# Kernel optimization log

Measured on AMD Instinct MI355X. Metric: run time of the kernel, lower is better.

The kernel has to match this reference:

```python
import jax, jax.numpy as jnp
import numpy as np

B, C, E = 2, 1024, 1024
H = 16            # n_heads as declared (used as per-group feature dim due to module's reshape)
HD = E // H       # 64 — the axis actually batched over in attention


def setup_inputs() -> dict:
    key = jax.random.key(0)
    ks = jax.random.split(key, 5)
    scale = 0.02
    return {
        "x": jax.random.normal(ks[0], (B, C, E), dtype=jnp.float32),
        "W_q": jax.random.normal(ks[1], (E, E), dtype=jnp.float32) * scale,
        "W_k": jax.random.normal(ks[2], (E, E), dtype=jnp.float32) * scale,
        "W_v": jax.random.normal(ks[3], (E, E), dtype=jnp.float32) * scale,
        "W_o": jax.random.normal(ks[4], (E, E), dtype=jnp.float32) * scale,
    }


def reference(x, W_q, W_k, W_v, W_o):
    # nn.Linear: y = x @ W.T  (bias=False)
    def proj_split(W):
        y = jnp.einsum('bce,de->bcd', x, W)              # [B,C,E]
        # view(B, C, HD, H).transpose(1,2) -> [B, HD, C, H]  (faithful to source layout)
        return y.reshape(B, C, HD, H).transpose(0, 2, 1, 3)

    Q = proj_split(W_q)
    K = proj_split(W_k)
    V = proj_split(W_v)

    scale = 1.0 / jnp.sqrt(jnp.asarray(H, dtype=x.dtype))  # sqrt of last dim (= n_heads here)
    scores = jnp.einsum('bdqh,bdkh->bdqk', Q, K) * scale    # [B, HD, C, C]
    weights = jax.nn.softmax(scores, axis=-1)
    out = jnp.einsum('bdqk,bdkh->bdqh', weights, V)         # [B, HD, C, H]
    out = out.transpose(0, 2, 1, 3).reshape(B, C, E)        # [B, C, E]
    out = jnp.einsum('bce,de->bcd', out, W_o)
    return out  # dropout p=0.0 / eval mode: identity
```

## Files before the change

### kernel.cpp

```cpp
#include <hip/hip_runtime.h>
#include <stdint.h>
#include <math.h>


typedef __bf16   bf16x8 __attribute__((ext_vector_type(8)));
typedef float    f32x4  __attribute__((ext_vector_type(4)));

__device__ __forceinline__ unsigned short f2bf(float f) {
    unsigned int u = __float_as_uint(f);
    u += 0x7FFFu + ((u >> 16) & 1u);
    return (unsigned short)(u >> 16);
}

__device__ __forceinline__ void gl16(const unsigned short* g, unsigned short* l) {
    __builtin_amdgcn_global_load_lds(
        (const __attribute__((address_space(1))) unsigned int*)g,
        (__attribute__((address_space(3))) unsigned int*)l, 16, 0, 0);
}

__global__ __launch_bounds__(256) void cast_to_bf16(
    const float* __restrict__ x,
    const float* __restrict__ w0, const float* __restrict__ w1,
    const float* __restrict__ w2, const float* __restrict__ w3,
    unsigned short* __restrict__ xb,
    unsigned short* __restrict__ b0, unsigned short* __restrict__ b1,
    unsigned short* __restrict__ b2, unsigned short* __restrict__ b3)
{
    const int z = blockIdx.y;
    const float* src;
    unsigned short* dst;
    size_t off = 0;
    float sc = 1.f;
    if (z < 2)       { src = x;  dst = xb; off = (size_t)z << 20; }
    else if (z == 2) { src = w0; dst = b0; sc = 0.36067376022224085f; }
    else if (z == 3) { src = w1; dst = b1; }
    else if (z == 4) { src = w2; dst = b2; }
    else             { src = w3; dst = b3; }
    const size_t i = off + ((size_t)blockIdx.x * 256 + threadIdx.x) * 4;
    const float4 v = *(const float4*)(src + i);
    *(ushort4*)(dst + i) = make_ushort4(f2bf(v.x * sc), f2bf(v.y * sc),
                                        f2bf(v.z * sc), f2bf(v.w * sc));
}

__global__ __launch_bounds__(256) void gemm128_bt_mfma(
    const unsigned short* __restrict__ A,
    const unsigned short* __restrict__ B0, const unsigned short* __restrict__ B1,
    const unsigned short* __restrict__ B2,
    unsigned short* __restrict__ C0, unsigned short* __restrict__ C1,
    unsigned short* __restrict__ C2,
    int M, int N, int K)
{
    const unsigned short* Bm = (blockIdx.z == 0) ? B0 : (blockIdx.z == 1) ? B1 : B2;
    unsigned short* Cm       = (blockIdx.z == 0) ? C0 : (blockIdx.z == 1) ? C1 : C2;

    __shared__ __align__(16) unsigned short As[2][128 * 32];
    __shared__ __align__(16) unsigned short Bs[2][128 * 32];

    const int t    = threadIdx.x;
    const int lane = t & 63;
    const int w    = t >> 6;
    const int m0   = blockIdx.y * 128;
    const int n0   = blockIdx.x * 128;
    const int wm   = (w & 1) * 64;
    const int wn   = (w >> 1) * 64;

    const int r0 = t >> 2;
    const int c0 = (t & 3) * 8;
    const unsigned short* Apa = A  + (size_t)(m0 + r0) * K + c0;
    const unsigned short* Apb = Apa + (size_t)64 * K;
    const unsigned short* Bpa = Bm + (size_t)(n0 + r0) * K + c0;
    const unsigned short* Bpb = Bpa + (size_t)64 * K;
    unsigned short* lA0 = &As[0][w * 512];
    unsigned short* lA1 = &As[0][2048 + w * 512];
    unsigned short* lB0 = &Bs[0][w * 512];
    unsigned short* lB1 = &Bs[0][2048 + w * 512];
    const int bufStr = 128 * 32;

    f32x4 acc[4][4];
#pragma unroll
    for (int i = 0; i < 4; ++i)
#pragma unroll
        for (int j = 0; j < 4; ++j) acc[i][j] = (f32x4){0.f, 0.f, 0.f, 0.f};

    const int fm = lane & 15;
    const int kg = lane >> 4;

    gl16(Apa, lA0);
    gl16(Apb, lA1);
    gl16(Bpa, lB0);
    gl16(Bpb, lB1);

    int cur = 0;
    for (int k0 = 0; k0 < K; k0 += 32) {
        __syncthreads();

        if (k0 + 32 < K) {
            const int nb = (cur ^ 1);
            gl16(Apa + k0 + 32, lA0 + nb * bufStr);
            gl16(Apb + k0 + 32, lA1 + nb * bufStr);
            gl16(Bpa + k0 + 32, lB0 + nb * bufStr);
            gl16(Bpb + k0 + 32, lB1 + nb * bufStr);
        }

        const unsigned short* Ab = &As[cur][0];
        const unsigned short* Bb = &Bs[cur][0];
        bf16x8 af[4], bfr[4];
#pragma unroll
        for (int im = 0; im < 4; ++im)
            af[im] = *(const bf16x8*)&Ab[(wm + im * 16 + fm) * 32 + kg * 8];
#pragma unroll
        for (int in = 0; in < 4; ++in)
            bfr[in] = *(const bf16x8*)&Bb[(wn + in * 16 + fm) * 32 + kg * 8];
#pragma unroll
        for (int im = 0; im < 4; ++im)
#pragma unroll
            for (int in = 0; in < 4; ++in)
                acc[im][in] = __builtin_amdgcn_mfma_f32_16x16x32_bf16(
                    af[im], bfr[in], acc[im][in], 0, 0, 0);

        cur ^= 1;
    }

#pragma unroll
    for (int im = 0; im < 4; ++im) {
#pragma unroll
        for (int in = 0; in < 4; ++in) {
            const int row = m0 + wm + im * 16 + kg * 4;
            const int col = n0 + wn + in * 16 + fm;
#pragma unroll
            for (int r = 0; r < 4; ++r)
                Cm[(size_t)(row + r) * N + col] = f2bf(acc[im][in][r]);
        }
    }
}

__global__ __launch_bounds__(256) void gemm64_bt_mfma(
    const unsigned short* __restrict__ A, const unsigned short* __restrict__ Bm,
    float* __restrict__ Cm, int M, int N, int K)
{
    __shared__ __align__(16) unsigned short As[2][64 * 32];
    __shared__ __align__(16) unsigned short Bs[2][64 * 32];

    const int t    = threadIdx.x;
    const int lane = t & 63;
    const int w    = t >> 6;
    const int m0   = blockIdx.y * 64;
    const int n0   = blockIdx.x * 64;
    const int wm   = (w & 1) * 32;
    const int wn   = (w >> 1) * 32;

    const int r0 = t >> 2;
    const int c0 = (t & 3) * 8;
    const unsigned short* Apa = A  + (size_t)(m0 + r0) * K + c0;
    const unsigned short* Bpa = Bm + (size_t)(n0 + r0) * K + c0;
    unsigned short* ldsA = &As[0][w * 512];
    unsigned short* ldsB = &Bs[0][w * 512];
    const int bufStr = 64 * 32;

    f32x4 acc[2][2];
#pragma unroll
    for (int i = 0; i < 2; ++i)
#pragma unroll
        for (int j = 0; j < 2; ++j) acc[i][j] = (f32x4){0.f, 0.f, 0.f, 0.f};

    const int fm = lane & 15;
    const int kg = lane >> 4;

    gl16(Apa, ldsA);
    gl16(Bpa, ldsB);

    int cur = 0;
    for (int k0 = 0; k0 < K; k0 += 32) {
        __syncthreads();

        if (k0 + 32 < K) {
            const int nb = (cur ^ 1);
            gl16(Apa + k0 + 32, ldsA + nb * bufStr);
            gl16(Bpa + k0 + 32, ldsB + nb * bufStr);
        }

        const unsigned short* Ab = &As[cur][0];
        const unsigned short* Bb = &Bs[cur][0];
        bf16x8 af[2], bfr[2];
#pragma unroll
        for (int im = 0; im < 2; ++im)
            af[im] = *(const bf16x8*)&Ab[(wm + im * 16 + fm) * 32 + kg * 8];
#pragma unroll
        for (int in = 0; in < 2; ++in)
            bfr[in] = *(const bf16x8*)&Bb[(wn + in * 16 + fm) * 32 + kg * 8];
#pragma unroll
        for (int im = 0; im < 2; ++im)
#pragma unroll
            for (int in = 0; in < 2; ++in)
                acc[im][in] = __builtin_amdgcn_mfma_f32_16x16x32_bf16(
                    af[im], bfr[in], acc[im][in], 0, 0, 0);

        cur ^= 1;
    }

#pragma unroll
    for (int im = 0; im < 2; ++im) {
#pragma unroll
        for (int in = 0; in < 2; ++in) {
            const int row = m0 + wm + im * 16 + kg * 4;
            const int col = n0 + wn + in * 16 + fm;
#pragma unroll
            for (int r = 0; r < 4; ++r)
                Cm[(size_t)(row + r) * N + col] = acc[im][in][r];
        }
    }
}

#define KROWS 40
#define VROWS 72

__global__ __launch_bounds__(256, 4) void attn_mfma(
    const unsigned short* __restrict__ Qb, const unsigned short* __restrict__ Kb,
    const unsigned short* __restrict__ Vb, unsigned short* __restrict__ Ob)
{
    __shared__ __align__(16) unsigned char smem[34816];

    const int t    = threadIdx.x;
    const int lane = t & 63;
    const int wv   = t >> 6;
    const int fm   = lane & 15;
    const int kg   = lane >> 4;

    const int blk = blockIdx.x;
    const int xcd = blk & 7;
    const int i_  = blk >> 3;
    const int qt  = i_ & 7;
    const int hdg = (i_ >> 3) & 3;
    const int gs  = (i_ >> 5) & 1;
    const int bb  = (i_ >> 6) & 1;
    const int hd  = (xcd + gs * 8) * 4 + hdg;
    const size_t base = ((size_t)bb << 20) + (size_t)hd * 16;
    const int q0 = qt * 128;
    const int wk = wv * 32;

    unsigned short* Ks  = (unsigned short*)(smem + wv * 2560);
    unsigned short* VsT = (unsigned short*)(smem + 10240 + wv * 2304);
    float*          Red = (float*)smem;

    const int key2 = lane >> 1, half = lane & 1;
    const int vcol = ((key2 & 15) >> 2) * 8 + (key2 & 3) + ((key2 >> 4) << 2);

    union { uint4 u; bf16x8 h; } zz; zz.u = make_uint4(0, 0, 0, 0);
    bf16x8 aq[8];
#pragma unroll
    for (int m = 0; m < 8; ++m) {
        if (kg < 2)
            aq[m] = *(const bf16x8*)(Qb + base +
                     (size_t)(q0 + m * 16 + fm) * 1024 + kg * 8);
        else
            aq[m] = zz.h;
    }

    f32x4 oacc[8];
    float lp[8];
#pragma unroll
    for (int m = 0; m < 8; ++m) {
        oacc[m] = (f32x4){0.f, 0.f, 0.f, 0.f};
        lp[m] = 0.f;
    }

    uint4 kd = *(const uint4*)(Kb + base + (size_t)(wk + key2) * 1024 + half * 8);
    uint4 vd = *(const uint4*)(Vb + base + (size_t)(wk + key2) * 1024 + half * 8);

    for (int kt = 0; kt < 1024; kt += 128) {
        {
            *(uint4*)&Ks[key2 * KROWS + half * 8] = kd;
            const unsigned short* pv = (const unsigned short*)&vd;
#pragma unroll
            for (int d = 0; d < 8; ++d)
                VsT[(half * 8 + d) * VROWS + vcol] = pv[d];
        }

        bf16x8 bk0 = zz.h, bk1 = zz.h;
        if (kg < 2) {
            bk0 = *(const bf16x8*)&Ks[fm * KROWS + kg * 8];
            bk1 = *(const bf16x8*)&Ks[(16 + fm) * KROWS + kg * 8];
        }

        const bf16x8 bv = *(const bf16x8*)&VsT[fm * VROWS + kg * 8];

        if (kt + 128 < 1024) {
            kd = *(const uint4*)(Kb + base +
                  (size_t)(kt + 128 + wk + key2) * 1024 + half * 8);
            vd = *(const uint4*)(Vb + base +
                  (size_t)(kt + 128 + wk + key2) * 1024 + half * 8);
        }

#pragma unroll
        for (int m = 0; m < 8; ++m) {
            f32x4 s0 = __builtin_amdgcn_mfma_f32_16x16x32_bf16(
                bk0, aq[m], (f32x4){0.f, 0.f, 0.f, 0.f}, 0, 0, 0);
            f32x4 s1 = __builtin_amdgcn_mfma_f32_16x16x32_bf16(
                bk1, aq[m], (f32x4){0.f, 0.f, 0.f, 0.f}, 0, 0, 0);
            const float p0 = __builtin_amdgcn_exp2f(s0[0]);
            const float p1 = __builtin_amdgcn_exp2f(s0[1]);
            const float p2 = __builtin_amdgcn_exp2f(s0[2]);
            const float p3 = __builtin_amdgcn_exp2f(s0[3]);
            const float p4 = __builtin_amdgcn_exp2f(s1[0]);
            const float p5 = __builtin_amdgcn_exp2f(s1[1]);
            const float p6 = __builtin_amdgcn_exp2f(s1[2]);
            const float p7 = __builtin_amdgcn_exp2f(s1[3]);
            lp[m] += ((p0 + p1) + (p2 + p3)) + ((p4 + p5) + (p6 + p7));
            bf16x8 aph;
            aph[0] = (__bf16)p0; aph[1] = (__bf16)p1;
            aph[2] = (__bf16)p2; aph[3] = (__bf16)p3;
            aph[4] = (__bf16)p4; aph[5] = (__bf16)p5;
            aph[6] = (__bf16)p6; aph[7] = (__bf16)p7;
            oacc[m] = __builtin_amdgcn_mfma_f32_16x16x32_bf16(
                aph, bv, oacc[m], 0, 0, 0);
        }
    }

#pragma unroll
    for (int m = 0; m < 8; ++m) {
        lp[m] += __shfl_xor(lp[m], 16, 64);
        lp[m] += __shfl_xor(lp[m], 32, 64);
    }

    __syncthreads();
#pragma unroll
    for (int m = 0; m < 8; ++m) {
#pragma unroll
        for (int r = 0; r < 4; ++r)
            Red[((wv * 128) + m * 16 + kg * 4 + r) * 17 + fm] = oacc[m][r];
        if (kg == 0)
            Red[((wv * 128) + m * 16 + fm) * 17 + 16] = lp[m];
    }
    __syncthreads();

#pragma unroll
    for (int mp = 0; mp < 2; ++mp) {
#pragma unroll
        for (int r = 0; r < 4; ++r) {
            const int q = wv * 32 + mp * 16 + kg * 4 + r;
            const float o = Red[q * 17 + fm]         + Red[(128 + q) * 17 + fm] +
                            Red[(256 + q) * 17 + fm] + Red[(384 + q) * 17 + fm];
            const float l = Red[q * 17 + 16]         + Red[(128 + q) * 17 + 16] +
                            Red[(256 + q) * 17 + 16] + Red[(384 + q) * 17 + 16];
            Ob[base + (size_t)(q0 + q) * 1024 + fm] = f2bf(o / l);
        }
    }
}

extern "C" void kernel_launch(void* const* d_in, const int* in_sizes, int n_in,
                              void* d_out, int out_size, void* d_ws, size_t ws_size,
                              hipStream_t stream) {
    const float* x  = (const float*)d_in[0];
    const float* Wq = (const float*)d_in[1];
    const float* Wk = (const float*)d_in[2];
    const float* Wv = (const float*)d_in[3];
    const float* Wo = (const float*)d_in[4];
    float* out = (float*)d_out;

    const int M = 2048, N = 1024, Kd = 1024;
    const size_t MEG = 1048576;
    unsigned short* ws = (unsigned short*)d_ws;
    unsigned short* xb  = ws;
    unsigned short* Wqb = ws + 2 * MEG;
    unsigned short* Wkb = ws + 3 * MEG;
    unsigned short* Wvb = ws + 4 * MEG;
    unsigned short* Wob = ws + 5 * MEG;
    unsigned short* Qb  = ws + 6 * MEG;
    unsigned short* Kb  = ws + 8 * MEG;
    unsigned short* Vb  = ws + 10 * MEG;
    unsigned short* Ob  = ws + 12 * MEG;

    dim3 gc(1024, 6, 1);
    cast_to_bf16<<<gc, 256, 0, stream>>>(x, Wq, Wk, Wv, Wo, xb, Wqb, Wkb, Wvb, Wob);

    dim3 g1(N / 128, M / 128, 3);
    gemm128_bt_mfma<<<g1, 256, 0, stream>>>(xb, Wqb, Wkb, Wvb, Qb, Kb, Vb, M, N, Kd);

    dim3 g2(1024, 1, 1);
    attn_mfma<<<g2, 256, 0, stream>>>(Qb, Kb, Vb, Ob);

    dim3 g3(N / 64, M / 64, 1);
    gemm64_bt_mfma<<<g3, 256, 0, stream>>>(Ob, Wob, out, M, N, Kd);
}
```

Baseline: 140.5 us.

## Use 128x64 QKV GEMM tiles and double-buffer K/V in attention LDS

The QKV projection GEMM now uses 128x64 output tiles instead of 128x128. This doubles the grid from 384 to 768 blocks for better CU occupancy on the 256-CU part, at the cost of more A-tile reloads. The attention kernel now double-buffers the per-wave K/V LDS tiles and preloads the next tile's fragments while computing the current one, aiming to hide LDS write/read latency. This grows shared memory per block and adds register pressure for the prefetched fragments.

```diff
diff --git a/kernel.cpp b/kernel.cpp
--- a/kernel.cpp
+++ b/kernel.cpp
@@ -42,7 +42,7 @@
                                         f2bf(v.z * sc), f2bf(v.w * sc));
 }
 
-__global__ __launch_bounds__(256) void gemm128_bt_mfma(
+__global__ __launch_bounds__(256) void gemm12864_bt_mfma(
     const unsigned short* __restrict__ A,
     const unsigned short* __restrict__ B0, const unsigned short* __restrict__ B1,
     const unsigned short* __restrict__ B2,
@@ -54,33 +54,32 @@
     unsigned short* Cm       = (blockIdx.z == 0) ? C0 : (blockIdx.z == 1) ? C1 : C2;
 
     __shared__ __align__(16) unsigned short As[2][128 * 32];
-    __shared__ __align__(16) unsigned short Bs[2][128 * 32];
+    __shared__ __align__(16) unsigned short Bs[2][64 * 32];
 
     const int t    = threadIdx.x;
     const int lane = t & 63;
     const int w    = t >> 6;
     const int m0   = blockIdx.y * 128;
-    const int n0   = blockIdx.x * 128;
+    const int n0   = blockIdx.x * 64;
     const int wm   = (w & 1) * 64;
-    const int wn   = (w >> 1) * 64;
+    const int wn   = (w >> 1) * 32;
 
     const int r0 = t >> 2;
     const int c0 = (t & 3) * 8;
     const unsigned short* Apa = A  + (size_t)(m0 + r0) * K + c0;
     const unsigned short* Apb = Apa + (size_t)64 * K;
     const unsigned short* Bpa = Bm + (size_t)(n0 + r0) * K + c0;
-    const unsigned short* Bpb = Bpa + (size_t)64 * K;
     unsigned short* lA0 = &As[0][w * 512];
     unsigned short* lA1 = &As[0][2048 + w * 512];
     unsigned short* lB0 = &Bs[0][w * 512];
-    unsigned short* lB1 = &Bs[0][2048 + w * 512];
-    const int bufStr = 128 * 32;
-
-    f32x4 acc[4][4];
+    const int bufStrA = 128 * 32;
+    const int bufStrB = 64 * 32;
+
+    f32x4 acc[4][2];
 #pragma unroll
     for (int i = 0; i < 4; ++i)
 #pragma unroll
-        for (int j = 0; j < 4; ++j) acc[i][j] = (f32x4){0.f, 0.f, 0.f, 0.f};
+        for (int j = 0; j < 2; ++j) acc[i][j] = (f32x4){0.f, 0.f, 0.f, 0.f};
 
     const int fm = lane & 15;
     const int kg = lane >> 4;
@@ -88,7 +87,6 @@
     gl16(Apa, lA0);
     gl16(Apb, lA1);
     gl16(Bpa, lB0);
-    gl16(Bpb, lB1);
 
     int cur = 0;
     for (int k0 = 0; k0 < K; k0 += 32) {
@@ -96,25 +94,24 @@
 
         if (k0 + 32 < K) {
             const int nb = (cur ^ 1);
-            gl16(Apa + k0 + 32, lA0 + nb * bufStr);
-            gl16(Apb + k0 + 32, lA1 + nb * bufStr);
-            gl16(Bpa + k0 + 32, lB0 + nb * bufStr);
-            gl16(Bpb + k0 + 32, lB1 + nb * bufStr);
+            gl16(Apa + k0 + 32, lA0 + nb * bufStrA);
+            gl16(Apb + k0 + 32, lA1 + nb * bufStrA);
+            gl16(Bpa + k0 + 32, lB0 + nb * bufStrB);
         }
 
         const unsigned short* Ab = &As[cur][0];
         const unsigned short* Bb = &Bs[cur][0];
-        bf16x8 af[4], bfr[4];
+        bf16x8 af[4], bfr[2];
 #pragma unroll
         for (int im = 0; im < 4; ++im)
             af[im] = *(const bf16x8*)&Ab[(wm + im * 16 + fm) * 32 + kg * 8];
 #pragma unroll
-        for (int in = 0; in < 4; ++in)
+        for (int in = 0; in < 2; ++in)
             bfr[in] = *(const bf16x8*)&Bb[(wn + in * 16 + fm) * 32 + kg * 8];
 #pragma unroll
         for (int im = 0; im < 4; ++im)
 #pragma unroll
-            for (int in = 0; in < 4; ++in)
+            for (int in = 0; in < 2; ++in)
                 acc[im][in] = __builtin_amdgcn_mfma_f32_16x16x32_bf16(
                     af[im], bfr[in], acc[im][in], 0, 0, 0);
 
@@ -124,7 +121,7 @@
 #pragma unroll
     for (int im = 0; im < 4; ++im) {
 #pragma unroll
-        for (int in = 0; in < 4; ++in) {
+        for (int in = 0; in < 2; ++in) {
             const int row = m0 + wm + im * 16 + kg * 4;
             const int col = n0 + wn + in * 16 + fm;
 #pragma unroll
@@ -218,7 +215,7 @@
     const unsigned short* __restrict__ Qb, const unsigned short* __restrict__ Kb,
     const unsigned short* __restrict__ Vb, unsigned short* __restrict__ Ob)
 {
-    __shared__ __align__(16) unsigned char smem[34816];
+    __shared__ __align__(16) unsigned char smem[38912];
 
     const int t    = threadIdx.x;
     const int lane = t & 63;
@@ -238,9 +235,9 @@
     const int q0 = qt * 128;
     const int wk = wv * 32;
 
-    unsigned short* Ks  = (unsigned short*)(smem + wv * 2560);
-    unsigned short* VsT = (unsigned short*)(smem + 10240 + wv * 2304);
-    float*          Red = (float*)smem;
+    unsigned short* Ks0  = (unsigned short*)(smem + wv * 5120);
+    unsigned short* VsT0 = (unsigned short*)(smem + 20480 + wv * 4608);
+    float*          Red  = (float*)smem;
 
     const int key2 = lane >> 1, half = lane & 1;
     const int vcol = ((key2 & 15) >> 2) * 8 + (key2 & 3) + ((key2 >> 4) << 2);
@@ -266,29 +263,47 @@
 
     uint4 kd = *(const uint4*)(Kb + base + (size_t)(wk + key2) * 1024 + half * 8);
     uint4 vd = *(const uint4*)(Vb + base + (size_t)(wk + key2) * 1024 + half * 8);
-
-    for (int kt = 0; kt < 1024; kt += 128) {
-        {
-            *(uint4*)&Ks[key2 * KROWS + half * 8] = kd;
+    {
+        *(uint4*)&Ks0[key2 * KROWS + half * 8] = kd;
+        const unsigned short* pv = (const unsigned short*)&vd;
+#pragma unroll
+        for (int d = 0; d < 8; ++d)
+            VsT0[(half * 8 + d) * VROWS + vcol] = pv[d];
+    }
+    kd = *(const uint4*)(Kb + base + (size_t)(128 + wk + key2) * 1024 + half * 8);
+    vd = *(const uint4*)(Vb + base + (size_t)(128 + wk + key2) * 1024 + half * 8);
+
+    bf16x8 bk0 = zz.h, bk1 = zz.h;
+    if (kg < 2) {
+        bk0 = *(const bf16x8*)&Ks0[fm * KROWS + kg * 8];
+        bk1 = *(const bf16x8*)&Ks0[(16 + fm) * KROWS + kg * 8];
+    }
+    bf16x8 bv = *(const bf16x8*)&VsT0[fm * VROWS + kg * 8];
+
+    int cur = 0;
+    for (int t8 = 0; t8 < 8; ++t8) {
+        bf16x8 nbk0 = zz.h, nbk1 = zz.h, nbv = zz.h;
+        if (t8 + 1 < 8) {
+            unsigned short* Kn = Ks0 + (cur ^ 1) * 1280;
+            unsigned short* Vn = VsT0 + (cur ^ 1) * 1152;
+            *(uint4*)&Kn[key2 * KROWS + half * 8] = kd;
             const unsigned short* pv = (const unsigned short*)&vd;
 #pragma unroll
             for (int d = 0; d < 8; ++d)
-                VsT[(half * 8 + d) * VROWS + vcol] = pv[d];
-        }
-
-        bf16x8 bk0 = zz.h, bk1 = zz.h;
-        if (kg < 2) {
-            bk0 = *(const bf16x8*)&Ks[fm * KROWS + kg * 8];
-            bk1 = *(const bf16x8*)&Ks[(16 + fm) * KROWS + kg * 8];
-        }
-
-        const bf16x8 bv = *(const bf16x8*)&VsT[fm * VROWS + kg * 8];
-
-        if (kt + 128 < 1024) {
-            kd = *(const uint4*)(Kb + base +
-                  (size_t)(kt + 128 + wk + key2) * 1024 + half * 8);
-            vd = *(const uint4*)(Vb + base +
-                  (size_t)(kt + 128 + wk + key2) * 1024 + half * 8);
+                Vn[(half * 8 + d) * VROWS + vcol] = pv[d];
+
+            if (t8 + 2 < 8) {
+                kd = *(const uint4*)(Kb + base +
+                      (size_t)((t8 + 2) * 128 + wk + key2) * 1024 + half * 8);
+                vd = *(const uint4*)(Vb + base +
+                      (size_t)((t8 + 2) * 128 + wk + key2) * 1024 + half * 8);
+            }
+
+            if (kg < 2) {
+                nbk0 = *(const bf16x8*)&Kn[fm * KROWS + kg * 8];
+                nbk1 = *(const bf16x8*)&Kn[(16 + fm) * KROWS + kg * 8];
+            }
+            nbv = *(const bf16x8*)&Vn[fm * VROWS + kg * 8];
         }
 
 #pragma unroll
@@ -314,6 +329,9 @@
             oacc[m] = __builtin_amdgcn_mfma_f32_16x16x32_bf16(
                 aph, bv, oacc[m], 0, 0, 0);
         }
+
+        bk0 = nbk0; bk1 = nbk1; bv = nbv;
+        cur ^= 1;
     }
 
 #pragma unroll
@@ -373,8 +391,8 @@
     dim3 gc(1024, 6, 1);
     cast_to_bf16<<<gc, 256, 0, stream>>>(x, Wq, Wk, Wv, Wo, xb, Wqb, Wkb, Wvb, Wob);
 
-    dim3 g1(N / 128, M / 128, 3);
-    gemm128_bt_mfma<<<g1, 256, 0, stream>>>(xb, Wqb, Wkb, Wvb, Qb, Kb, Vb, M, N, Kd);
+    dim3 g1(N / 64, M / 128, 3);
+    gemm12864_bt_mfma<<<g1, 256, 0, stream>>>(xb, Wqb, Wkb, Wvb, Qb, Kb, Vb, M, N, Kd);
 
     dim3 g2(1024, 1, 1);
     attn_mfma<<<g2, 256, 0, stream>>>(Qb, Kb, Vb, Ob);
```

New measurement: 152.8 us. 1.09x slower.
